# Performance work log

Hardware: AMD Instinct MI355X
Metric: run time of the kernel (lower is better)

Reference implementation:

```python
import jax, jax.numpy as jnp
import numpy as np

N_USERS = 200000
N_ITEMS = 100000
EMBED_DIM = 64
N_LAYERS = 3
N_INTER = 1000000


def setup_inputs() -> dict:
    key = jax.random.key(0)
    k1, k2, k3, k4 = jax.random.split(key, 4)
    user_ids = jax.random.randint(k1, (N_INTER,), 0, N_USERS, dtype=jnp.int64 if jax.config.jax_enable_x64 else jnp.int32)
    item_ids = jax.random.randint(k2, (N_INTER,), 0, N_ITEMS, dtype=jnp.int64 if jax.config.jax_enable_x64 else jnp.int32)
    user_emb = jax.random.normal(k3, (N_USERS, EMBED_DIM), dtype=jnp.float32) * 0.1
    item_emb = jax.random.normal(k4, (N_ITEMS, EMBED_DIM), dtype=jnp.float32) * 0.1
    return {"user_emb": user_emb, "item_emb": item_emb, "user_ids": user_ids, "item_ids": item_ids}


def reference(user_emb, item_emb, user_ids, item_ids):
    n_users = user_emb.shape[0]
    n_items = item_emb.shape[0]
    n_nodes = n_users + n_items

    # Symmetric bipartite adjacency as directed edge list (both directions).
    src = jnp.concatenate([user_ids, item_ids + n_users])   # [2E]
    dst = jnp.concatenate([item_ids + n_users, user_ids])   # [2E]

    # Symmetric normalization D^{-1/2} A D^{-1/2} (duplicate edges sum, matching scipy CSR).
    deg = jax.ops.segment_sum(jnp.ones_like(src, dtype=jnp.float32), src, num_segments=n_nodes)
    d_inv_sqrt = jnp.where(deg > 0, jax.lax.rsqrt(jnp.maximum(deg, 1.0)), 0.0)
    w = d_inv_sqrt[src] * d_inv_sqrt[dst]                    # [2E] edge weights

    emb = jnp.concatenate([user_emb, item_emb], axis=0)      # [n_nodes, d]
    acc = emb
    for _ in range(N_LAYERS):
        # SpMM: out[dst] += w * emb[src]
        emb = jax.ops.segment_sum(w[:, None] * emb[src], dst, num_segments=n_nodes)
        acc = acc + emb
    final = acc / (N_LAYERS + 1)                             # mean over stacked layers
    return final[:n_users], final[n_users:]
```

## Files before the change

kernel.cpp:

```cpp
#include <hip/hip_runtime.h>

#define N_USERS 200000
#define N_ITEMS 100000
#define N_NODES 300000
#define DIM 64
#define N_INTER 1000000

#define BSHIFT 10
#define BNODES (1 << BSHIFT)
#define NBUCKET ((N_NODES + BNODES - 1) >> BSHIFT)
#define TILE 4096
#define NBLK_P ((N_INTER + TILE - 1) / TILE)

typedef unsigned short bf16_t;
typedef unsigned int u32;

static __device__ __forceinline__ bf16_t f2bf(float f) {
    union { float f; u32 u; } v; v.f = f;
    u32 r = v.u + 0x7FFFu + ((v.u >> 16) & 1u);
    return (bf16_t)(r >> 16);
}
static __device__ __forceinline__ float bf2f(bf16_t h) {
    union { u32 u; float f; } v; v.u = ((u32)h) << 16;
    return v.f;
}

__global__ void hist_kernel(const int* __restrict__ uid, const int* __restrict__ iid,
                            u32* __restrict__ bucket_count) {
    __shared__ u32 h[NBUCKET];
    int t = threadIdx.x;
    for (int i = t; i < NBUCKET; i += 256) h[i] = 0;
    __syncthreads();
    int base = blockIdx.x * TILE;
    int end = base + TILE; if (end > N_INTER) end = N_INTER;
    for (int k = base + t; k < end; k += 256) {
        int u = uid[k];
        int it = N_USERS + iid[k];
        atomicAdd(&h[it >> BSHIFT], 1u);
        atomicAdd(&h[u >> BSHIFT], 1u);
    }
    __syncthreads();
    for (int i = t; i < NBUCKET; i += 256)
        if (h[i]) atomicAdd(&bucket_count[i], h[i]);
}

__global__ void scan_kernel(const u32* __restrict__ bucket_count, u32* __restrict__ bstart,
                            u32* __restrict__ bucket_cursor, u32* __restrict__ rowptr) {
    __shared__ u32 buf[2][512];
    int t = threadIdx.x;
    u32 v0 = (t < NBUCKET) ? bucket_count[t] : 0u;
    buf[0][t] = v0;
    __syncthreads();
    int s = 0;
    for (int off = 1; off < 512; off <<= 1) {
        u32 v = buf[s][t];
        if (t >= off) v += buf[s][t - off];
        buf[1 - s][t] = v;
        __syncthreads();
        s = 1 - s;
    }
    if (t < NBUCKET) {
        u32 excl = buf[s][t] - v0;
        bstart[t] = excl;
        bucket_cursor[t] = excl;
    }
    if (t == 0) {
        bstart[NBUCKET] = 2 * N_INTER;
        rowptr[N_NODES] = 2 * N_INTER;
    }
}

__global__ void place_kernel(const int* __restrict__ uid, const int* __restrict__ iid,
                             u32* __restrict__ bucket_cursor, u32* __restrict__ bdata) {
    __shared__ u32 h[NBUCKET];
    __shared__ u32 basesh[NBUCKET];
    int t = threadIdx.x;
    for (int i = t; i < NBUCKET; i += 256) h[i] = 0;
    __syncthreads();
    int base = blockIdx.x * TILE;
    int end = base + TILE; if (end > N_INTER) end = N_INTER;
    for (int k = base + t; k < end; k += 256) {
        int u = uid[k];
        int it = N_USERS + iid[k];
        atomicAdd(&h[it >> BSHIFT], 1u);
        atomicAdd(&h[u >> BSHIFT], 1u);
    }
    __syncthreads();
    for (int i = t; i < NBUCKET; i += 256) {
        u32 c = h[i];
        basesh[i] = c ? atomicAdd(&bucket_cursor[i], c) : 0u;
        h[i] = 0;
    }
    __syncthreads();
    for (int k = base + t; k < end; k += 256) {
        int u = uid[k];
        int it = N_USERS + iid[k];
        {
            int b = it >> BSHIFT;
            u32 pos = basesh[b] + atomicAdd(&h[b], 1u);
            bdata[pos] = (((u32)(it & (BNODES - 1))) << 19) | (u32)u;
        }
        {
            int b = u >> BSHIFT;
            u32 pos = basesh[b] + atomicAdd(&h[b], 1u);
            bdata[pos] = (((u32)(u & (BNODES - 1))) << 19) | (u32)it;
        }
    }
}

__global__ void csr_kernel(const u32* __restrict__ bstart, const u32* __restrict__ bdata,
                           u32* __restrict__ rowptr, float* __restrict__ dinv,
                           int* __restrict__ col) {
    __shared__ u32 cnt[BNODES];
    __shared__ u32 sb[2][BNODES];
    __shared__ u32 cur[BNODES];
    int b = blockIdx.x;
    int t = threadIdx.x;
    int nbase = b << BSHIFT;
    u32 bs = bstart[b], be = bstart[b + 1];
    u32 m = be - bs;

    #pragma unroll
    for (int j = 0; j < 4; ++j) cnt[t + j * 256] = 0;
    __syncthreads();
    for (u32 e = t; e < m; e += 256) {
        u32 v = bdata[bs + e];
        atomicAdd(&cnt[v >> 19], 1u);
    }
    __syncthreads();
    #pragma unroll
    for (int j = 0; j < 4; ++j) sb[0][t + j * 256] = cnt[t + j * 256];
    __syncthreads();
    int s = 0;
    for (int off = 1; off < BNODES; off <<= 1) {
        #pragma unroll
        for (int j = 0; j < 4; ++j) {
            int idx = t + j * 256;
            u32 v = sb[s][idx];
            if (idx >= off) v += sb[s][idx - off];
            sb[1 - s][idx] = v;
        }
        __syncthreads();
        s = 1 - s;
    }
    #pragma unroll
    for (int j = 0; j < 4; ++j) {
        int idx = t + j * 256;
        int node = nbase + idx;
        u32 c = cnt[idx];
        u32 excl = sb[s][idx] - c;
        cur[idx] = excl;
        if (node < N_NODES) {
            rowptr[node] = bs + excl;
            dinv[node] = (c > 0) ? rsqrtf((float)c) : 0.0f;
        }
    }
    __syncthreads();
    for (u32 e = t; e < m; e += 256) {
        u32 v = bdata[bs + e];
        u32 ln = v >> 19;
        u32 pos = atomicAdd(&cur[ln], 1u);
        col[bs + pos] = (int)(v & 0x7FFFFu);
    }
}

__global__ void ecol_kernel(const int* __restrict__ col, const float* __restrict__ dinv,
                            int2* __restrict__ ecol) {
    int e = blockIdx.x * blockDim.x + threadIdx.x;
    if (e < 2 * N_INTER) {
        int s = col[e];
        ecol[e] = make_int2(s, __float_as_int(dinv[s]));
    }
}

__global__ void init_kernel(const float4* __restrict__ ue, const float4* __restrict__ ie,
                            ushort4* __restrict__ cur) {
    int idx = blockIdx.x * blockDim.x + threadIdx.x;
    if (idx < N_NODES * 16) {
        float4 v = (idx < N_USERS * 16) ? ue[idx] : ie[idx - N_USERS * 16];
        ushort4 h;
        h.x = f2bf(v.x); h.y = f2bf(v.y); h.z = f2bf(v.z); h.w = f2bf(v.w);
        cur[idx] = h;
    }
}

__global__ void gather_kernel(const u32* __restrict__ rowptr, const int2* __restrict__ ecol,
                              const float* __restrict__ dinv,
                              const bf16_t* __restrict__ cur, bf16_t* __restrict__ nxt) {
    int n = (blockIdx.x * blockDim.x + threadIdx.x) >> 6;
    int lane = threadIdx.x & 63;
    n = __builtin_amdgcn_readfirstlane(n);
    if (n >= N_NODES) return;
    u32 start = rowptr[n], end = rowptr[n + 1];
    float acc = 0.0f;
    for (u32 base = start; base < end; base += 64) {
        int cnt = (int)(end - base); if (cnt > 64) cnt = 64;
        int2 e = make_int2(0, 0);
        if (lane < cnt) e = ecol[base + lane];
        for (int j = 0; j < cnt; j += 8) {
            int s[8], w[8];
            #pragma unroll
            for (int k = 0; k < 8; ++k) {
                int lidx = __builtin_amdgcn_readfirstlane(j + k);
                s[k] = __builtin_amdgcn_readlane(e.x, lidx);
                w[k] = __builtin_amdgcn_readlane(e.y, lidx);
            }
            float r[8];
            #pragma unroll
            for (int k = 0; k < 8; ++k)
                r[k] = bf2f(cur[((u32)s[k] << 6) + lane]);
            #pragma unroll
            for (int k = 0; k < 8; ++k)
                acc += __int_as_float(w[k]) * r[k];
        }
    }
    nxt[((u32)n << 6) + lane] = f2bf(dinv[n] * acc);
}

__global__ void gather_final_kernel(const u32* __restrict__ rowptr, const int2* __restrict__ ecol,
                                    const float* __restrict__ dinv,
                                    const bf16_t* __restrict__ b1, const bf16_t* __restrict__ b2,
                                    const float* __restrict__ ue, const float* __restrict__ ie,
                                    float* __restrict__ out) {
    int n = (blockIdx.x * blockDim.x + threadIdx.x) >> 6;
    int lane = threadIdx.x & 63;
    n = __builtin_amdgcn_readfirstlane(n);
    if (n >= N_NODES) return;
    u32 start = rowptr[n], end = rowptr[n + 1];
    float acc = 0.0f;
    for (u32 base = start; base < end; base += 64) {
        int cnt = (int)(end - base); if (cnt > 64) cnt = 64;
        int2 e = make_int2(0, 0);
        if (lane < cnt) e = ecol[base + lane];
        for (int j = 0; j < cnt; j += 8) {
            int s[8], w[8];
            #pragma unroll
            for (int k = 0; k < 8; ++k) {
                int lidx = __builtin_amdgcn_readfirstlane(j + k);
                s[k] = __builtin_amdgcn_readlane(e.x, lidx);
                w[k] = __builtin_amdgcn_readlane(e.y, lidx);
            }
            float r[8];
            #pragma unroll
            for (int k = 0; k < 8; ++k)
                r[k] = bf2f(b2[((u32)s[k] << 6) + lane]);
            #pragma unroll
            for (int k = 0; k < 8; ++k)
                acc += __int_as_float(w[k]) * r[k];
        }
    }
    float r = dinv[n] * acc;
    u32 o = ((u32)n << 6) + lane;
    float e0 = (n < N_USERS) ? ue[o] : ie[o - (u32)N_USERS * DIM];
    out[o] = (e0 + bf2f(b1[o]) + bf2f(b2[o]) + r) * 0.25f;
}

extern "C" void kernel_launch(void* const* d_in, const int* in_sizes, int n_in,
                              void* d_out, int out_size, void* d_ws, size_t ws_size,
                              hipStream_t stream) {
    const float* ue = (const float*)d_in[0];
    const float* ie = (const float*)d_in[1];
    const int* uid = (const int*)d_in[2];
    const int* iid = (const int*)d_in[3];
    float* out = (float*)d_out;

    char* ws = (char*)d_ws;
    size_t off = 0;
    auto alloc = [&](size_t bytes) { char* p = ws + off; off = (off + bytes + 255) & ~(size_t)255; return p; };
    u32*    bucket_count  = (u32*)alloc((size_t)NBUCKET * 4);
    u32*    bstart        = (u32*)alloc((size_t)(NBUCKET + 1) * 4);
    u32*    bucket_cursor = (u32*)alloc((size_t)NBUCKET * 4);
    u32*    rowptr        = (u32*)alloc((size_t)(N_NODES + 1) * 4);
    float*  dinv          = (float*)alloc((size_t)N_NODES * 4);
    u32*    bdata         = (u32*)alloc((size_t)2 * N_INTER * 4);
    int*    col           = (int*)alloc((size_t)2 * N_INTER * 4);
    int2*   ecol          = (int2*)alloc((size_t)2 * N_INTER * 8);
    bf16_t* buf0          = (bf16_t*)alloc((size_t)N_NODES * DIM * 2);
    bf16_t* buf1          = (bf16_t*)alloc((size_t)N_NODES * DIM * 2);
    bf16_t* buf2          = (bf16_t*)alloc((size_t)N_NODES * DIM * 2);

    hipMemsetAsync(bucket_count, 0, (size_t)NBUCKET * 4, stream);
    hist_kernel<<<NBLK_P, 256, 0, stream>>>(uid, iid, bucket_count);
    scan_kernel<<<1, 512, 0, stream>>>(bucket_count, bstart, bucket_cursor, rowptr);
    place_kernel<<<NBLK_P, 256, 0, stream>>>(uid, iid, bucket_cursor, bdata);
    csr_kernel<<<NBUCKET, 256, 0, stream>>>(bstart, bdata, rowptr, dinv, col);
    ecol_kernel<<<(2 * N_INTER + 255) / 256, 256, 0, stream>>>(col, dinv, ecol);

    init_kernel<<<(N_NODES * 16 + 255) / 256, 256, 0, stream>>>(
        (const float4*)ue, (const float4*)ie, (ushort4*)buf0);

    gather_kernel<<<(N_NODES * 64 + 255) / 256, 256, 0, stream>>>(rowptr, ecol, dinv, buf0, buf1);
    gather_kernel<<<(N_NODES * 64 + 255) / 256, 256, 0, stream>>>(rowptr, ecol, dinv, buf1, buf2);
    gather_final_kernel<<<(N_NODES * 64 + 255) / 256, 256, 0, stream>>>(
        rowptr, ecol, dinv, buf1, buf2, ue, ie, out);
}
```

Before: 454.6 us.

## Process eight consecutive nodes per wavefront in SpMM gather kernels

Each wavefront now handles eight consecutive CSR rows instead of one. It loads the nine row pointers once and streams the shared edge range in 64-edge chunks that can span row boundaries. The goal is to cut per-wave launch and setup overhead and to make fuller use of each ecol load, since the average degree is only about 6.7. In exchange the inner loop becomes serialized per-edge with predicated tail handling, and there are 8x fewer waves, which lowers the memory-level parallelism available to hide gather latency.

```diff
diff --git a/kernel.cpp b/kernel.cpp
--- a/kernel.cpp
+++ b/kernel.cpp
@@ -11,6 +11,10 @@
 #define NBUCKET ((N_NODES + BNODES - 1) >> BSHIFT)
 #define TILE 4096
 #define NBLK_P ((N_INTER + TILE - 1) / TILE)
+
+#define NPW 8
+#define NWAVE ((N_NODES + NPW - 1) / NPW)
+#define GATHER_THREADS (NWAVE * 64)
 
 typedef unsigned short bf16_t;
 typedef unsigned int u32;
@@ -187,34 +191,49 @@
 __global__ void gather_kernel(const u32* __restrict__ rowptr, const int2* __restrict__ ecol,
                               const float* __restrict__ dinv,
                               const bf16_t* __restrict__ cur, bf16_t* __restrict__ nxt) {
-    int n = (blockIdx.x * blockDim.x + threadIdx.x) >> 6;
+    int wid = (blockIdx.x * blockDim.x + threadIdx.x) >> 6;
     int lane = threadIdx.x & 63;
-    n = __builtin_amdgcn_readfirstlane(n);
-    if (n >= N_NODES) return;
-    u32 start = rowptr[n], end = rowptr[n + 1];
-    float acc = 0.0f;
-    for (u32 base = start; base < end; base += 64) {
-        int cnt = (int)(end - base); if (cnt > 64) cnt = 64;
-        int2 e = make_int2(0, 0);
-        if (lane < cnt) e = ecol[base + lane];
-        for (int j = 0; j < cnt; j += 8) {
-            int s[8], w[8];
-            #pragma unroll
-            for (int k = 0; k < 8; ++k) {
-                int lidx = __builtin_amdgcn_readfirstlane(j + k);
-                s[k] = __builtin_amdgcn_readlane(e.x, lidx);
-                w[k] = __builtin_amdgcn_readlane(e.y, lidx);
+    int n0 = __builtin_amdgcn_readfirstlane(wid * NPW);
+    if (n0 >= N_NODES) return;
+    u32 rp[NPW + 1];
+    #pragma unroll
+    for (int i = 0; i <= NPW; ++i) rp[i] = rowptr[n0 + i];
+    u32 eend = rp[NPW];
+    u32 cbase = rp[0];
+    int2 e = make_int2(0, 0);
+    {
+        u32 cc = eend - cbase; if (cc > 64) cc = 64;
+        if ((u32)lane < cc) e = ecol[cbase + lane];
+    }
+    u32 pos = rp[0];
+    #pragma unroll
+    for (int r = 0; r < NPW; ++r) {
+        u32 re = rp[r + 1];
+        float acc = 0.0f;
+        while (pos < re) {
+            u32 cend = cbase + 64;
+            u32 lim = re < cend ? re : cend;
+            for (u32 p = pos; p < lim; p += 8) {
+                #pragma unroll
+                for (int k = 0; k < 8; ++k) {
+                    u32 ei = p + (u32)k;
+                    int lidx = (ei < lim) ? (int)(ei - cbase) : 0;
+                    lidx = __builtin_amdgcn_readfirstlane(lidx);
+                    int s = __builtin_amdgcn_readlane(e.x, lidx);
+                    int wb = (ei < lim) ? __builtin_amdgcn_readlane(e.y, lidx) : 0;
+                    acc += __int_as_float(wb) * bf2f(cur[((u32)s << 6) + lane]);
+                }
             }
-            float r[8];
-            #pragma unroll
-            for (int k = 0; k < 8; ++k)
-                r[k] = bf2f(cur[((u32)s[k] << 6) + lane]);
-            #pragma unroll
-            for (int k = 0; k < 8; ++k)
-                acc += __int_as_float(w[k]) * r[k];
-        }
-    }
-    nxt[((u32)n << 6) + lane] = f2bf(dinv[n] * acc);
+            pos = lim;
+            if (pos == cend && pos < eend) {
+                cbase = pos;
+                u32 cc = eend - cbase; if (cc > 64) cc = 64;
+                e = make_int2(0, 0);
+                if ((u32)lane < cc) e = ecol[cbase + lane];
+            }
+        }
+        nxt[(((u32)(n0 + r)) << 6) + (u32)lane] = f2bf(dinv[n0 + r] * acc);
+    }
 }
 
 __global__ void gather_final_kernel(const u32* __restrict__ rowptr, const int2* __restrict__ ecol,
@@ -222,37 +241,53 @@
                                     const bf16_t* __restrict__ b1, const bf16_t* __restrict__ b2,
                                     const float* __restrict__ ue, const float* __restrict__ ie,
                                     float* __restrict__ out) {
-    int n = (blockIdx.x * blockDim.x + threadIdx.x) >> 6;
+    int wid = (blockIdx.x * blockDim.x + threadIdx.x) >> 6;
     int lane = threadIdx.x & 63;
-    n = __builtin_amdgcn_readfirstlane(n);
-    if (n >= N_NODES) return;
-    u32 start = rowptr[n], end = rowptr[n + 1];
-    float acc = 0.0f;
-    for (u32 base = start; base < end; base += 64) {
-        int cnt = (int)(end - base); if (cnt > 64) cnt = 64;
-        int2 e = make_int2(0, 0);
-        if (lane < cnt) e = ecol[base + lane];
-        for (int j = 0; j < cnt; j += 8) {
-            int s[8], w[8];
-            #pragma unroll
-            for (int k = 0; k < 8; ++k) {
-                int lidx = __builtin_amdgcn_readfirstlane(j + k);
-                s[k] = __builtin_amdgcn_readlane(e.x, lidx);
-                w[k] = __builtin_amdgcn_readlane(e.y, lidx);
+    int n0 = __builtin_amdgcn_readfirstlane(wid * NPW);
+    if (n0 >= N_NODES) return;
+    u32 rp[NPW + 1];
+    #pragma unroll
+    for (int i = 0; i <= NPW; ++i) rp[i] = rowptr[n0 + i];
+    u32 eend = rp[NPW];
+    u32 cbase = rp[0];
+    int2 e = make_int2(0, 0);
+    {
+        u32 cc = eend - cbase; if (cc > 64) cc = 64;
+        if ((u32)lane < cc) e = ecol[cbase + lane];
+    }
+    u32 pos = rp[0];
+    #pragma unroll
+    for (int r = 0; r < NPW; ++r) {
+        u32 re = rp[r + 1];
+        float acc = 0.0f;
+        while (pos < re) {
+            u32 cend = cbase + 64;
+            u32 lim = re < cend ? re : cend;
+            for (u32 p = pos; p < lim; p += 8) {
+                #pragma unroll
+                for (int k = 0; k < 8; ++k) {
+                    u32 ei = p + (u32)k;
+                    int lidx = (ei < lim) ? (int)(ei - cbase) : 0;
+                    lidx = __builtin_amdgcn_readfirstlane(lidx);
+                    int s = __builtin_amdgcn_readlane(e.x, lidx);
+                    int wb = (ei < lim) ? __builtin_amdgcn_readlane(e.y, lidx) : 0;
+                    acc += __int_as_float(wb) * bf2f(b2[((u32)s << 6) + lane]);
+                }
             }
-            float r[8];
-            #pragma unroll
-            for (int k = 0; k < 8; ++k)
-                r[k] = bf2f(b2[((u32)s[k] << 6) + lane]);
-            #pragma unroll
-            for (int k = 0; k < 8; ++k)
-                acc += __int_as_float(w[k]) * r[k];
-        }
-    }
-    float r = dinv[n] * acc;
-    u32 o = ((u32)n << 6) + lane;
-    float e0 = (n < N_USERS) ? ue[o] : ie[o - (u32)N_USERS * DIM];
-    out[o] = (e0 + bf2f(b1[o]) + bf2f(b2[o]) + r) * 0.25f;
+            pos = lim;
+            if (pos == cend && pos < eend) {
+                cbase = pos;
+                u32 cc = eend - cbase; if (cc > 64) cc = 64;
+                e = make_int2(0, 0);
+                if ((u32)lane < cc) e = ecol[cbase + lane];
+            }
+        }
+        int n = n0 + r;
+        float rr = dinv[n] * acc;
+        u32 o = (((u32)n) << 6) + (u32)lane;
+        float e0 = (n < N_USERS) ? ue[o] : ie[o - (u32)N_USERS * DIM];
+        out[o] = (e0 + bf2f(b1[o]) + bf2f(b2[o]) + rr) * 0.25f;
+    }
 }
 
 extern "C" void kernel_launch(void* const* d_in, const int* in_sizes, int n_in,
@@ -289,8 +324,8 @@
     init_kernel<<<(N_NODES * 16 + 255) / 256, 256, 0, stream>>>(
         (const float4*)ue, (const float4*)ie, (ushort4*)buf0);
 
-    gather_kernel<<<(N_NODES * 64 + 255) / 256, 256, 0, stream>>>(rowptr, ecol, dinv, buf0, buf1);
-    gather_kernel<<<(N_NODES * 64 + 255) / 256, 256, 0, stream>>>(rowptr, ecol, dinv, buf1, buf2);
-    gather_final_kernel<<<(N_NODES * 64 + 255) / 256, 256, 0, stream>>>(
+    gather_kernel<<<(GATHER_THREADS + 255) / 256, 256, 0, stream>>>(rowptr, ecol, dinv, buf0, buf1);
+    gather_kernel<<<(GATHER_THREADS + 255) / 256, 256, 0, stream>>>(rowptr, ecol, dinv, buf1, buf2);
+    gather_final_kernel<<<(GATHER_THREADS + 255) / 256, 256, 0, stream>>>(
         rowptr, ecol, dinv, buf1, buf2, ue, ie, out);
 }
```

New measurement: 424.5 us. 6.6% less time.
